# Kernel optimization log

Hardware: AMD Instinct MI355X
Metric: run time of the kernel (lower is better)

Reference implementation:

```python
import jax, jax.numpy as jnp
import numpy as np

P = 16          # patch size
IMG = 384       # image size
D = 768         # model dim
DM = 3072       # mlp hidden
L = 12          # n blocks
H = 12          # n heads
DH = D // H     # head dim
NC = 1000       # n classes
B = 64          # batch
N = (IMG // P) ** 2  # 576 patches


def layernorm(x, w, b, eps=1e-5):
    m = jnp.mean(x, axis=-1, keepdims=True)
    v = jnp.mean((x - m) ** 2, axis=-1, keepdims=True)
    return (x - m) / jnp.sqrt(v + eps) * w + b


def gelu(x):
    return jax.nn.gelu(x, approximate=False)  # torch nn.GELU default (erf)


def setup_inputs() -> dict:
    key = jax.random.key(0)
    ks = iter(jax.random.split(key, 40))
    nrm = lambda shape, s=0.02: jax.random.normal(next(ks), shape, jnp.float32) * s
    return {
        "x": jax.random.normal(next(ks), (B, 3, IMG, IMG), jnp.float32),
        "class_embed": nrm((D,)),
        "pose_embed": nrm((N + 1, D)),
        "proj_w": nrm((3 * P * P, D)), "proj_b": jnp.zeros((D,), jnp.float32),
        "qkv_w": nrm((L, D, 3 * D)), "qkv_b": jnp.zeros((L, 3 * D), jnp.float32),
        "top_w": nrm((L, D, D)), "top_b": jnp.zeros((L, D), jnp.float32),
        "ln1_w": jnp.ones((L, D), jnp.float32), "ln1_b": jnp.zeros((L, D), jnp.float32),
        "ln2_w": jnp.ones((L, D), jnp.float32), "ln2_b": jnp.zeros((L, D), jnp.float32),
        "mlp_w1": nrm((L, D, DM)), "mlp_b1": jnp.zeros((L, DM), jnp.float32),
        "mlp_w2": nrm((L, DM, D)), "mlp_b2": jnp.zeros((L, D), jnp.float32),
        "ln3_w": jnp.ones((D,), jnp.float32), "ln3_b": jnp.zeros((D,), jnp.float32),
        "head_w1": nrm((D, DM)), "head_b1": jnp.zeros((DM,), jnp.float32),
        "head_w2": nrm((DM, NC)), "head_b2": jnp.zeros((NC,), jnp.float32),
    }


def reference(x, class_embed, pose_embed, proj_w, proj_b, qkv_w, qkv_b,
              top_w, top_b, ln1_w, ln1_b, ln2_w, ln2_b,
              mlp_w1, mlp_b1, mlp_w2, mlp_b2, ln3_w, ln3_b,
              head_w1, head_b1, head_w2, head_b2):
    Bx = x.shape[0]
    # _slice_patch: torch unfold(dim2).unfold(dim3) -> (B,C,N,P,P) -> permute -> flatten (C,Ph,Pw order)
    patches = x.reshape(Bx, 3, IMG // P, P, IMG // P, P)
    patches = patches.transpose(0, 2, 4, 1, 3, 5).reshape(Bx, N, 3 * P * P)
    patch_embed = patches @ proj_w + proj_b  # (B, N, D)
    cls = jnp.broadcast_to(class_embed, (Bx, 1, D))
    z = jnp.concatenate([cls, patch_embed], axis=1) + pose_embed  # (B, N+1, D)

    scale = DH ** 0.5
    for i in range(L):
        # MSA branch (note: source computes attention over the HEAD axis per token, HxH)
        h = layernorm(z, ln1_w[i], ln1_b[i])
        qkv = h @ qkv_w[i] + qkv_b[i]
        q, k, v = jnp.split(qkv, 3, axis=-1)
        q = q.reshape(Bx, N + 1, H, DH)
        k = k.reshape(Bx, N + 1, H, DH)
        v = v.reshape(Bx, N + 1, H, DH)
        A = jax.nn.softmax(jnp.einsum('bnhd,bngd->bnhg', q, k) / scale, axis=-1)
        o = jnp.einsum('bnhg,bngd->bnhd', A, v).reshape(Bx, N + 1, D)
        z = o @ top_w[i] + top_b[i] + z
        # MLP branch (GELU after both linears, per source MLP)
        h2 = layernorm(z, ln2_w[i], ln2_b[i])
        m = gelu(gelu(h2 @ mlp_w1[i] + mlp_b1[i]) @ mlp_w2[i] + mlp_b2[i])
        z = m + z

    y = layernorm(z[:, 0], ln3_w, ln3_b)  # (B, D)
    logit = gelu(gelu(y @ head_w1 + head_b1) @ head_w2 + head_b2)  # pretraining cls_head = MLP
    return logit
```

## Files before the change

kernel.cpp:

```cpp
#include <hip/hip_runtime.h>

typedef unsigned short u16;
typedef unsigned int u32;
typedef __bf16 bf16x8 __attribute__((ext_vector_type(8)));
typedef float f32x4 __attribute__((ext_vector_type(4)));

#define D_    768
#define DM_   3072
#define NL_   12
#define NT_   577
#define NP_   576
#define B_    64
#define MREAL (B_*NT_)
#define MPAD2 37120
#define NC_   1000
#define IMG_  384

__device__ __forceinline__ float bf2f(u16 v){
  union { unsigned u; float f; } c; c.u = ((unsigned)v) << 16; return c.f;
}
__device__ __forceinline__ u16 f2bf(float f){
  union { float f; unsigned u; } c; c.f = f;
  unsigned r = c.u + 0x7FFFu + ((c.u >> 16) & 1u);
  return (u16)(r >> 16);
}
__device__ __forceinline__ float gelu_f(float x){
  return 0.5f * x * (1.0f + erff(x * 0.70710678118654752f));
}
__device__ __forceinline__ void gload16(const void* g, void* l){
  __builtin_amdgcn_global_load_lds((const __attribute__((address_space(1))) void*)g,
                                   (__attribute__((address_space(3))) void*)l, 16, 0, 0);
}

template<int EPI>
__global__ __launch_bounds__(512, 1) void gemm256_k(
    const u16* __restrict__ A, const u16* __restrict__ Bt,
    const float* __restrict__ bias, const float* __restrict__ res,
    void* __restrict__ outv, int K, int ldo, int nbn)
{
  __shared__ u16 lds[2][2][256*64];
  const int tid = threadIdx.x;
  const int l   = tid & 63;
  const int wid = tid >> 6;
  const int wm  = wid >> 2, wn = wid & 3;
  const int lrow = l & 15;

  const int nwg = gridDim.x;
  const int q = nwg >> 3, r = nwg & 7;
  const int xcd = blockIdx.x & 7, o = blockIdx.x >> 3;
  const int wg = (xcd < r ? xcd * (q + 1) : r * (q + 1) + (xcd - r) * q) + o;
  const int bm = wg / nbn, bn = wg % nbn;

  const int cs8 = ((tid & 7) ^ ((tid >> 3) & 7)) * 8;
  const int rb  = tid >> 3;
  const u16* aP[4]; const u16* bP[4];
  #pragma unroll
  for (int i = 0; i < 4; i++) {
    aP[i] = A  + (size_t)(bm*256 + rb + 64*i) * K + cs8;
    bP[i] = Bt + (size_t)(bn*256 + rb + 64*i) * K + cs8;
  }
  const int ldst = tid * 8;

  f32x4 acc[8][4];
  #pragma unroll
  for (int i = 0; i < 8; i++)
    #pragma unroll
    for (int j = 0; j < 4; j++) acc[i][j] = {0.f, 0.f, 0.f, 0.f};

  const int nk = K >> 6;
  #pragma unroll
  for (int i = 0; i < 4; i++) {
    gload16(aP[i], &lds[0][0][ldst + i*4096]);
    gload16(bP[i], &lds[0][1][ldst + i*4096]);
    aP[i] += 64; bP[i] += 64;
  }

  const int sw  = (lrow & 7) << 4;
  const int g16 = (l >> 4) << 4;

  for (int t = 0; t < nk; ++t) {
    const int cur = t & 1;
    if (t + 1 < nk) {
      #pragma unroll
      for (int i = 0; i < 4; i++) {
        gload16(aP[i], &lds[cur^1][0][ldst + i*4096]);
        gload16(bP[i], &lds[cur^1][1][ldst + i*4096]);
        aP[i] += 64; bP[i] += 64;
      }
      __builtin_amdgcn_sched_barrier(0);
      asm volatile("s_waitcnt vmcnt(8)" ::: "memory");
    } else {
      __builtin_amdgcn_sched_barrier(0);
      asm volatile("s_waitcnt vmcnt(0)" ::: "memory");
    }
    __builtin_amdgcn_sched_barrier(0);
    __builtin_amdgcn_s_barrier();
    __builtin_amdgcn_sched_barrier(0);
    const char* As_ = (const char*)&lds[cur][0][0];
    const char* Bs_ = (const char*)&lds[cur][1][0];
    #pragma unroll
    for (int kk = 0; kk < 2; kk++) {
      bf16x8 af[8], bfr[4];
      const int kb = (kk << 6) | g16;
      #pragma unroll
      for (int mi = 0; mi < 8; mi++)
        af[mi] = *(const bf16x8*)(As_ + ((wm*128 + mi*16 + lrow) << 7) + (kb ^ sw));
      #pragma unroll
      for (int ni = 0; ni < 4; ni++)
        bfr[ni] = *(const bf16x8*)(Bs_ + ((wn*64 + ni*16 + lrow) << 7) + (kb ^ sw));
      #pragma unroll
      for (int mi = 0; mi < 8; mi++)
        #pragma unroll
        for (int ni = 0; ni < 4; ni++)
          acc[mi][ni] = __builtin_amdgcn_mfma_f32_16x16x32_bf16(af[mi], bfr[ni], acc[mi][ni], 0, 0, 0);
    }
    __builtin_amdgcn_sched_barrier(0);
    __builtin_amdgcn_s_barrier();
    __builtin_amdgcn_sched_barrier(0);
  }

  const int orow0 = bm*256 + wm*128;
  const int ocol0 = bn*256 + wn*64;
  #pragma unroll
  for (int mi = 0; mi < 8; mi++) {
    #pragma unroll
    for (int ni = 0; ni < 4; ni++) {
      const int col = ocol0 + ni*16 + (l & 15);
      const float bv = bias[col];
      #pragma unroll
      for (int r2 = 0; r2 < 4; r2++) {
        const int row = orow0 + mi*16 + (l >> 4)*4 + r2;
        const float v = acc[mi][ni][r2] + bv;
        const size_t idx = (size_t)row * ldo + col;
        if constexpr (EPI == 0) ((u16*)outv)[idx] = f2bf(v);
        else if constexpr (EPI == 1) ((float*)outv)[idx] = v + res[idx];
        else if constexpr (EPI == 2) ((u16*)outv)[idx] = f2bf(gelu_f(v));
        else if constexpr (EPI == 3) ((float*)outv)[idx] = gelu_f(v) + res[idx];
        else if constexpr (EPI == 4) ((float*)outv)[idx] = v;
      }
    }
  }
}

template<int EPI>
__global__ __launch_bounds__(256) void gemm_k(
    const u16* __restrict__ A, const u16* __restrict__ Bt,
    const float* __restrict__ bias, const float* __restrict__ res,
    void* __restrict__ outv, int K, int ldo, int nbn, int Ms, int Ns)
{
  __shared__ u16 As[128*64];
  __shared__ u16 Bs[128*64];
  const int tid = threadIdx.x;
  const int l   = tid & 63;
  const int w   = tid >> 6;
  const int wm  = w >> 1, wn = w & 1;
  const int lrow = l & 15;

  const int nwg = gridDim.x;
  const int q = nwg >> 3, r = nwg & 7;
  const int xcd = blockIdx.x & 7, o = blockIdx.x >> 3;
  const int wg = (xcd < r ? xcd * (q + 1) : r * (q + 1) + (xcd - r) * q) + o;
  const int bm = wg / nbn, bn = wg % nbn;

  const int cs8 = ((tid & 7) ^ ((tid >> 3) & 7)) * 8;
  const int rb  = tid >> 3;
  const size_t abase = (size_t)bm * 128 * K;
  const size_t bbase = (size_t)bn * 128 * K;
  size_t aoff[4], boff[4];
  #pragma unroll
  for (int i = 0; i < 4; i++) {
    aoff[i] = abase + (size_t)(rb + 32 * i) * K + cs8;
    boff[i] = bbase + (size_t)(rb + 32 * i) * K + cs8;
  }

  const int colA = (l >> 4) << 4;
  const int sw   = (lrow & 7) << 4;

  f32x4 acc[4][4];
  #pragma unroll
  for (int i = 0; i < 4; i++)
    #pragma unroll
    for (int j = 0; j < 4; j++) acc[i][j] = {0.f, 0.f, 0.f, 0.f};

  const int nk = K >> 6;
  for (int kt = 0; kt < nk; ++kt) {
    const int koff = kt * 64;
    #pragma unroll
    for (int i = 0; i < 4; i++) {
      gload16(A  + aoff[i] + koff, As + tid * 8 + i * 2048);
      gload16(Bt + boff[i] + koff, Bs + tid * 8 + i * 2048);
    }
    __syncthreads();
    #pragma unroll
    for (int kk = 0; kk < 2; kk++) {
      bf16x8 af[4], bfr[4];
      #pragma unroll
      for (int mi = 0; mi < 4; mi++)
        af[mi] = *(const bf16x8*)((const char*)As +
                  ((wm*64 + mi*16 + lrow) << 7) + (((kk << 6) | colA) ^ sw));
      #pragma unroll
      for (int ni = 0; ni < 4; ni++)
        bfr[ni] = *(const bf16x8*)((const char*)Bs +
                  ((wn*64 + ni*16 + lrow) << 7) + (((kk << 6) | colA) ^ sw));
      #pragma unroll
      for (int mi = 0; mi < 4; mi++)
        #pragma unroll
        for (int ni = 0; ni < 4; ni++)
          acc[mi][ni] = __builtin_amdgcn_mfma_f32_16x16x32_bf16(af[mi], bfr[ni], acc[mi][ni], 0, 0, 0);
    }
    __syncthreads();
  }

  const int orow0 = bm*128 + wm*64;
  const int ocol0 = bn*128 + wn*64;
  #pragma unroll
  for (int mi = 0; mi < 4; mi++) {
    #pragma unroll
    for (int ni = 0; ni < 4; ni++) {
      #pragma unroll
      for (int r2 = 0; r2 < 4; r2++) {
        const int row = orow0 + mi*16 + (l >> 4)*4 + r2;
        const int col = ocol0 + ni*16 + (l & 15);
        float bv;
        if constexpr (EPI == 5) bv = (col < Ns) ? bias[col] : 0.f;
        else bv = bias[col];
        const float v = acc[mi][ni][r2] + bv;
        const size_t idx = (size_t)row * ldo + col;
        if constexpr (EPI == 2) ((u16*)outv)[idx] = f2bf(gelu_f(v));
        else if constexpr (EPI == 5) {
          if (row < Ms && col < Ns) ((float*)outv)[(size_t)row * Ns + col] = gelu_f(v);
        }
      }
    }
  }
}

__global__ void wconv_k(const float* __restrict__ W, u16* __restrict__ Wt,
                        int K, int N)
{
  __shared__ float tile[32][33];
  const int n0 = blockIdx.x * 32, k0 = blockIdx.y * 32;
  const int tx = threadIdx.x, ty = threadIdx.y;
  #pragma unroll
  for (int r = 0; r < 4; r++) {
    const int kk = k0 + ty + r*8;
    const int nn = n0 + tx;
    tile[ty + r*8][tx] = (nn < N) ? W[(size_t)kk * N + nn] : 0.f;
  }
  __syncthreads();
  #pragma unroll
  for (int r = 0; r < 4; r++) {
    const int nn = n0 + ty + r*8;
    Wt[(size_t)nn * K + k0 + tx] = f2bf(tile[tx][ty + r*8]);
  }
}

__global__ void patchify_k(const float* __restrict__ x, u16* __restrict__ hb)
{
  const int blk = blockIdx.x;
  const int b = blk / NP_, p = blk % NP_;
  const int pr = p / 24, pc = p % 24;
  const size_t row = (size_t)b * NT_ + 1 + p;
  #pragma unroll
  for (int u = 0; u < 3; u++) {
    const int j  = threadIdx.x + u * 256;
    const int c  = j >> 8, ph = (j >> 4) & 15, pw = j & 15;
    const float v = x[((size_t)(b*3 + c) * IMG_ + pr*16 + ph) * IMG_ + pc*16 + pw];
    hb[row * D_ + j] = f2bf(v);
  }
}

__global__ void posecls_k(float* __restrict__ z, const float* __restrict__ ce,
                          const float* __restrict__ pe)
{
  const int row = blockIdx.x;
  const int t = row % NT_;
  const size_t base = (size_t)row * D_;
  #pragma unroll
  for (int u = 0; u < 3; u++) {
    const int j = threadIdx.x + u * 256;
    if (t == 0) z[base + j] = ce[j] + pe[j];
    else        z[base + j] += pe[(size_t)t * D_ + j];
  }
}

__global__ void ln_k(const float* __restrict__ z, const float* __restrict__ w,
                     const float* __restrict__ b, u16* __restrict__ out)
{
  const int row = blockIdx.x * 4 + (threadIdx.x >> 6);
  const int l = threadIdx.x & 63;
  const float4* zr = (const float4*)(z + (size_t)row * D_);
  float4 xq[3];
  float s = 0.f;
  #pragma unroll
  for (int j = 0; j < 3; j++) {
    xq[j] = zr[j*64 + l];
    s += xq[j].x + xq[j].y + xq[j].z + xq[j].w;
  }
  #pragma unroll
  for (int m = 1; m < 64; m <<= 1) s += __shfl_xor(s, m, 64);
  const float mean = s * (1.0f / 768.0f);
  float ss = 0.f;
  #pragma unroll
  for (int j = 0; j < 3; j++) {
    const float dx = xq[j].x-mean, dy = xq[j].y-mean, dz = xq[j].z-mean, dw = xq[j].w-mean;
    ss += dx*dx + dy*dy + dz*dz + dw*dw;
  }
  #pragma unroll
  for (int m = 1; m < 64; m <<= 1) ss += __shfl_xor(ss, m, 64);
  const float rinv = rsqrtf(ss * (1.0f / 768.0f) + 1e-5f);
  const size_t ob = (size_t)row * D_;
  #pragma unroll
  for (int j = 0; j < 3; j++) {
    const int c = (j*64 + l) * 4;
    const float4 wv = *(const float4*)(w + c);
    const float4 bv = *(const float4*)(b + c);
    ushort4 ov;
    ov.x = f2bf((xq[j].x - mean) * rinv * wv.x + bv.x);
    ov.y = f2bf((xq[j].y - mean) * rinv * wv.y + bv.y);
    ov.z = f2bf((xq[j].z - mean) * rinv * wv.z + bv.z);
    ov.w = f2bf((xq[j].w - mean) * rinv * wv.w + bv.w);
    *(ushort4*)(out + ob + c) = ov;
  }
}

__global__ void lncls_k(const float* __restrict__ z, const float* __restrict__ w,
                        const float* __restrict__ b, u16* __restrict__ out)
{
  const int row = blockIdx.x * 4 + (threadIdx.x >> 6);
  const int l = threadIdx.x & 63;
  const size_t ob = (size_t)row * D_;
  if (row >= B_) {
    #pragma unroll
    for (int j = 0; j < 12; j++) out[ob + j*64 + l] = 0;
    return;
  }
  const float* zr = z + (size_t)row * NT_ * D_;
  float xv[12];
  float s = 0.f;
  #pragma unroll
  for (int j = 0; j < 12; j++) { xv[j] = zr[j*64 + l]; s += xv[j]; }
  #pragma unroll
  for (int m = 1; m < 64; m <<= 1) s += __shfl_xor(s, m, 64);
  const float mean = s * (1.0f / 768.0f);
  float ss = 0.f;
  #pragma unroll
  for (int j = 0; j < 12; j++) { const float d = xv[j] - mean; ss += d * d; }
  #pragma unroll
  for (int m = 1; m < 64; m <<= 1) ss += __shfl_xor(ss, m, 64);
  const float rinv = rsqrtf(ss * (1.0f / 768.0f) + 1e-5f);
  #pragma unroll
  for (int j = 0; j < 12; j++) {
    const int cidx = j*64 + l;
    out[ob + cidx] = f2bf((xv[j] - mean) * rinv * w[cidx] + b[cidx]);
  }
}

__global__ __launch_bounds__(256) void attn_k(const u16* __restrict__ qkv,
                                              u16* __restrict__ o)
{
  const int tok = (blockIdx.x * 256 + threadIdx.x) >> 6;
  const int l  = threadIdx.x & 63;
  const int g  = l >> 4, li = l & 15;
  const size_t rb = (size_t)tok * (3 * D_);

  f32x4 s = {0.f, 0.f, 0.f, 0.f};
  #pragma unroll
  for (int kt = 0; kt < 2; kt++) {
    const bf16x8 ka = *(const bf16x8*)(qkv + rb + D_ + li*64 + g*8 + kt*32);
    const bf16x8 qb = *(const bf16x8*)(qkv + rb +      li*64 + g*8 + kt*32);
    s = __builtin_amdgcn_mfma_f32_16x16x32_bf16(ka, qb, s, 0, 0, 0);
  }

  float sv[4];
  #pragma unroll
  for (int r2 = 0; r2 < 4; r2++) sv[r2] = s[r2] * 0.125f;
  float mx = (g < 3) ? fmaxf(fmaxf(sv[0], sv[1]), fmaxf(sv[2], sv[3])) : -1e30f;
  mx = fmaxf(mx, __shfl_xor(mx, 16, 64));
  mx = fmaxf(mx, __shfl_xor(mx, 32, 64));
  float p[4], den = 0.f;
  #pragma unroll
  for (int r2 = 0; r2 < 4; r2++) {
    p[r2] = (g < 3) ? __expf(sv[r2] - mx) : 0.f;
    den += p[r2];
  }
  den += __shfl_xor(den, 16, 64);
  den += __shfl_xor(den, 32, 64);
  const float rden = 1.0f / den;
  #pragma unroll
  for (int r2 = 0; r2 < 4; r2++) p[r2] *= rden;

  const u32 pk01 = ((u32)f2bf(p[1]) << 16) | f2bf(p[0]);
  const u32 pk23 = ((u32)f2bf(p[3]) << 16) | f2bf(p[2]);

  const int srcA = (li + (g << 5)) & 63;
  const int srcB = (srcA + 16) & 63;
  u32 b0 = (u32)__shfl((int)pk01, srcA, 64);
  u32 b1 = (u32)__shfl((int)pk23, srcA, 64);
  u32 b2 = (u32)__shfl((int)pk01, srcB, 64);
  u32 b3 = (u32)__shfl((int)pk23, srcB, 64);
  if (g >= 2) { b0 = 0; b1 = 0; b2 = 0; b3 = 0; }
  union { u32 u[4]; bf16x8 v; } pb;
  pb.u[0] = b0; pb.u[1] = b1; pb.u[2] = b2; pb.u[3] = b3;

  const size_t ob = (size_t)tok * D_;
  #pragma unroll
  for (int t = 0; t < 4; t++) {
    union { u16 a[8]; bf16x8 v; } va;
    #pragma unroll
    for (int jp = 0; jp < 8; jp++) {
      const int j = g * 8 + jp;
      va.a[jp] = (j < 12) ? qkv[rb + 2*D_ + j*64 + t*16 + li] : (u16)0;
    }
    f32x4 oac = {0.f, 0.f, 0.f, 0.f};
    oac = __builtin_amdgcn_mfma_f32_16x16x32_bf16(va.v, pb.v, oac, 0, 0, 0);
    if (li < 12) {
      ushort4 ov;
      ov.x = f2bf(oac[0]); ov.y = f2bf(oac[1]);
      ov.z = f2bf(oac[2]); ov.w = f2bf(oac[3]);
      *(ushort4*)(o + ob + li*64 + t*16 + g*4) = ov;
    }
  }
}

extern "C" void kernel_launch(void* const* d_in, const int* in_sizes, int n_in,
                              void* d_out, int out_size, void* d_ws, size_t ws_size,
                              hipStream_t stream)
{
  const float* x    = (const float*)d_in[0];
  const float* ce   = (const float*)d_in[1];
  const float* pe   = (const float*)d_in[2];
  const float* pw   = (const float*)d_in[3];
  const float* pb   = (const float*)d_in[4];
  const float* qkvw = (const float*)d_in[5];
  const float* qkvb = (const float*)d_in[6];
  const float* topw = (const float*)d_in[7];
  const float* topb = (const float*)d_in[8];
  const float* l1w  = (const float*)d_in[9];
  const float* l1b  = (const float*)d_in[10];
  const float* l2w  = (const float*)d_in[11];
  const float* l2b  = (const float*)d_in[12];
  const float* w1   = (const float*)d_in[13];
  const float* b1   = (const float*)d_in[14];
  const float* w2   = (const float*)d_in[15];
  const float* b2   = (const float*)d_in[16];
  const float* l3w  = (const float*)d_in[17];
  const float* l3b  = (const float*)d_in[18];
  const float* hw1  = (const float*)d_in[19];
  const float* hb1  = (const float*)d_in[20];
  const float* hw2  = (const float*)d_in[21];
  const float* hb2  = (const float*)d_in[22];

  char* ws = (char*)d_ws;
  constexpr size_t SZ_Z  = (size_t)MPAD2 * D_ * 4;
  constexpr size_t SZ_HB = (size_t)MPAD2 * D_ * 2;
  constexpr size_t SZ_QM = (size_t)MPAD2 * DM_ * 2;
  constexpr size_t SZ_WB = (size_t)DM_ * 1024 * 2;
  constexpr size_t SZ_YB = (size_t)128 * D_ * 2;
  float* z  = (float*)ws;
  u16*   hb = (u16*)(ws + SZ_Z);
  u16*   qm = (u16*)(ws + SZ_Z + SZ_HB);
  u16*   wb = (u16*)(ws + SZ_Z + SZ_HB + SZ_QM);
  u16*   yb = (u16*)(ws + SZ_Z + SZ_HB + SZ_QM + SZ_WB);
  u16*   t1 = (u16*)(ws + SZ_Z + SZ_HB + SZ_QM + SZ_WB + SZ_YB);

  const dim3 blk(256);
  const dim3 blk5(512);
  const dim3 wblk(32, 8);
  const int MT2 = MPAD2 / 256;

  patchify_k<<<B_ * NP_, blk, 0, stream>>>(x, hb);
  wconv_k<<<dim3(D_/32, D_/32), wblk, 0, stream>>>(pw, wb, D_, D_);
  gemm256_k<4><<<3*MT2, blk5, 0, stream>>>(hb, wb, pb, nullptr, z, D_, D_, 3);
  posecls_k<<<MREAL, blk, 0, stream>>>(z, ce, pe);

  for (int i = 0; i < NL_; i++) {
    ln_k<<<MPAD2/4, blk, 0, stream>>>(z, l1w + i*D_, l1b + i*D_, hb);
    wconv_k<<<dim3(3*D_/32, D_/32), wblk, 0, stream>>>(qkvw + (size_t)i*D_*3*D_, wb, D_, 3*D_);
    gemm256_k<0><<<9*MT2, blk5, 0, stream>>>(hb, wb, qkvb + i*3*D_, nullptr, qm, D_, 3*D_, 9);
    attn_k<<<MREAL/4, blk, 0, stream>>>(qm, hb);
    wconv_k<<<dim3(D_/32, D_/32), wblk, 0, stream>>>(topw + (size_t)i*D_*D_, wb, D_, D_);
    gemm256_k<1><<<3*MT2, blk5, 0, stream>>>(hb, wb, topb + i*D_, z, z, D_, D_, 3);
    ln_k<<<MPAD2/4, blk, 0, stream>>>(z, l2w + i*D_, l2b + i*D_, hb);
    wconv_k<<<dim3(DM_/32, D_/32), wblk, 0, stream>>>(w1 + (size_t)i*D_*DM_, wb, D_, DM_);
    gemm256_k<2><<<12*MT2, blk5, 0, stream>>>(hb, wb, b1 + i*DM_, nullptr, qm, D_, DM_, 12);
    wconv_k<<<dim3(D_/32, DM_/32), wblk, 0, stream>>>(w2 + (size_t)i*DM_*D_, wb, DM_, D_);
    gemm256_k<3><<<3*MT2, blk5, 0, stream>>>(qm, wb, b2 + i*D_, z, z, DM_, D_, 3);
  }

  lncls_k<<<32, blk, 0, stream>>>(z, l3w, l3b, yb);
  wconv_k<<<dim3(DM_/32, D_/32), wblk, 0, stream>>>(hw1, wb, D_, DM_);
  gemm_k<2><<<24, blk, 0, stream>>>(yb, wb, hb1, nullptr, t1, D_, DM_, 24, 0, 0);
  wconv_k<<<dim3(1024/32, DM_/32), wblk, 0, stream>>>(hw2, wb, DM_, NC_);
  gemm_k<5><<<8, blk, 0, stream>>>(t1, wb, hb2, nullptr, (float*)d_out, DM_, 1024, 8, B_, NC_);
}
```

Measured before the change: 11.85 ms.

## Interleave global prefetch with MFMA phases in GEMM main loop

The GEMM K-loop is split into four sub-phases, each of two M-halves by two K-halves. Each phase loads its A/B fragments from LDS and issues part of the next tile's global-to-LDS prefetch, then raises wave priority around its MFMA block. The aim is to spread memory traffic across the compute, overlap it better, and reduce fragment register pressure (af goes from 8 to 4). The trade-off is four workgroup barriers per K-step instead of two, plus stricter lgkmcnt waits, which could add synchronisation stalls.

```diff
diff --git a/kernel.cpp b/kernel.cpp
--- a/kernel.cpp
+++ b/kernel.cpp
@@ -32,6 +32,8 @@
                                    (__attribute__((address_space(3))) void*)l, 16, 0, 0);
 }
 
+#define SB_ __builtin_amdgcn_sched_barrier(0)
+
 template<int EPI>
 __global__ __launch_bounds__(512, 1) void gemm256_k(
     const u16* __restrict__ A, const u16* __restrict__ Bt,
@@ -80,43 +82,119 @@
 
   for (int t = 0; t < nk; ++t) {
     const int cur = t & 1;
-    if (t + 1 < nk) {
-      #pragma unroll
-      for (int i = 0; i < 4; i++) {
-        gload16(aP[i], &lds[cur^1][0][ldst + i*4096]);
-        gload16(bP[i], &lds[cur^1][1][ldst + i*4096]);
-        aP[i] += 64; bP[i] += 64;
-      }
-      __builtin_amdgcn_sched_barrier(0);
-      asm volatile("s_waitcnt vmcnt(8)" ::: "memory");
-    } else {
-      __builtin_amdgcn_sched_barrier(0);
-      asm volatile("s_waitcnt vmcnt(0)" ::: "memory");
-    }
-    __builtin_amdgcn_sched_barrier(0);
+    const bool pre = (t + 1 < nk);
+    u16* dA = &lds[cur^1][0][0];
+    u16* dB = &lds[cur^1][1][0];
+
+    if (pre) {
+      gload16(aP[0], dA + ldst);
+      gload16(aP[1], dA + ldst + 4096);
+    }
+    SB_;
+    if (pre) asm volatile("s_waitcnt vmcnt(2)" ::: "memory");
+    else     asm volatile("s_waitcnt vmcnt(0)" ::: "memory");
+    SB_;
     __builtin_amdgcn_s_barrier();
-    __builtin_amdgcn_sched_barrier(0);
+    SB_;
+
     const char* As_ = (const char*)&lds[cur][0][0];
     const char* Bs_ = (const char*)&lds[cur][1][0];
-    #pragma unroll
-    for (int kk = 0; kk < 2; kk++) {
-      bf16x8 af[8], bfr[4];
-      const int kb = (kk << 6) | g16;
-      #pragma unroll
-      for (int mi = 0; mi < 8; mi++)
-        af[mi] = *(const bf16x8*)(As_ + ((wm*128 + mi*16 + lrow) << 7) + (kb ^ sw));
+    bf16x8 af[4], bfr[4];
+
+    {
+      const int kb = g16;
       #pragma unroll
       for (int ni = 0; ni < 4; ni++)
         bfr[ni] = *(const bf16x8*)(Bs_ + ((wn*64 + ni*16 + lrow) << 7) + (kb ^ sw));
       #pragma unroll
-      for (int mi = 0; mi < 8; mi++)
+      for (int mi = 0; mi < 4; mi++)
+        af[mi] = *(const bf16x8*)(As_ + ((wm*128 + mi*16 + lrow) << 7) + (kb ^ sw));
+      if (pre) {
+        gload16(aP[2], dA + ldst + 8192);
+        gload16(aP[3], dA + ldst + 12288);
+      }
+      asm volatile("s_waitcnt lgkmcnt(0)" ::: "memory");
+      SB_;
+      __builtin_amdgcn_s_setprio(1);
+      #pragma unroll
+      for (int mi = 0; mi < 4; mi++)
         #pragma unroll
         for (int ni = 0; ni < 4; ni++)
           acc[mi][ni] = __builtin_amdgcn_mfma_f32_16x16x32_bf16(af[mi], bfr[ni], acc[mi][ni], 0, 0, 0);
-    }
-    __builtin_amdgcn_sched_barrier(0);
-    __builtin_amdgcn_s_barrier();
-    __builtin_amdgcn_sched_barrier(0);
+      __builtin_amdgcn_s_setprio(0);
+      SB_;
+      __builtin_amdgcn_s_barrier();
+      SB_;
+    }
+    {
+      const int kb = g16;
+      #pragma unroll
+      for (int mi = 0; mi < 4; mi++)
+        af[mi] = *(const bf16x8*)(As_ + ((wm*128 + (mi+4)*16 + lrow) << 7) + (kb ^ sw));
+      if (pre) {
+        gload16(bP[0], dB + ldst);
+        gload16(bP[1], dB + ldst + 4096);
+      }
+      asm volatile("s_waitcnt lgkmcnt(0)" ::: "memory");
+      SB_;
+      __builtin_amdgcn_s_setprio(1);
+      #pragma unroll
+      for (int mi = 0; mi < 4; mi++)
+        #pragma unroll
+        for (int ni = 0; ni < 4; ni++)
+          acc[mi+4][ni] = __builtin_amdgcn_mfma_f32_16x16x32_bf16(af[mi], bfr[ni], acc[mi+4][ni], 0, 0, 0);
+      __builtin_amdgcn_s_setprio(0);
+      SB_;
+      __builtin_amdgcn_s_barrier();
+      SB_;
+    }
+    {
+      const int kb = 64 | g16;
+      #pragma unroll
+      for (int ni = 0; ni < 4; ni++)
+        bfr[ni] = *(const bf16x8*)(Bs_ + ((wn*64 + ni*16 + lrow) << 7) + (kb ^ sw));
+      #pragma unroll
+      for (int mi = 0; mi < 4; mi++)
+        af[mi] = *(const bf16x8*)(As_ + ((wm*128 + mi*16 + lrow) << 7) + (kb ^ sw));
+      if (pre) {
+        gload16(bP[2], dB + ldst + 8192);
+        gload16(bP[3], dB + ldst + 12288);
+      }
+      asm volatile("s_waitcnt lgkmcnt(0)" ::: "memory");
+      SB_;
+      __builtin_amdgcn_s_setprio(1);
+      #pragma unroll
+      for (int mi = 0; mi < 4; mi++)
+        #pragma unroll
+        for (int ni = 0; ni < 4; ni++)
+          acc[mi][ni] = __builtin_amdgcn_mfma_f32_16x16x32_bf16(af[mi], bfr[ni], acc[mi][ni], 0, 0, 0);
+      __builtin_amdgcn_s_setprio(0);
+      SB_;
+      __builtin_amdgcn_s_barrier();
+      SB_;
+    }
+    {
+      const int kb = 64 | g16;
+      #pragma unroll
+      for (int mi = 0; mi < 4; mi++)
+        af[mi] = *(const bf16x8*)(As_ + ((wm*128 + (mi+4)*16 + lrow) << 7) + (kb ^ sw));
+      asm volatile("s_waitcnt lgkmcnt(0)" ::: "memory");
+      SB_;
+      __builtin_amdgcn_s_setprio(1);
+      #pragma unroll
+      for (int mi = 0; mi < 4; mi++)
+        #pragma unroll
+        for (int ni = 0; ni < 4; ni++)
+          acc[mi+4][ni] = __builtin_amdgcn_mfma_f32_16x16x32_bf16(af[mi], bfr[ni], acc[mi+4][ni], 0, 0, 0);
+      __builtin_amdgcn_s_setprio(0);
+      SB_;
+      __builtin_amdgcn_s_barrier();
+      SB_;
+    }
+    if (pre) {
+      #pragma unroll
+      for (int i = 0; i < 4; i++) { aP[i] += 64; bP[i] += 64; }
+    }
   }
 
   const int orow0 = bm*256 + wm*128;
```

Measured after the change: 11.24 ms. 5.2% less time.

## Add 128x128 GEMM kernel for N=768 projections and raise MFMA priority

Applied to the files above, without the earlier changes.

Adds a 128x128-tile, 256-thread GEMM variant with two workgroups per CU and uses it for the patch embedding, attention output projection and MLP down-projection, where N=768 produced only 3 column tiles and a small grid. The 256-tile kernel is kept for the QKV and MLP up-projections, now without the residual epilogues. Both kernels replace the sched_barrier-wrapped barriers with a plain inline s_barrier and raise wave priority around the MFMA section with s_setprio. Smaller tiles give more workgroups and better CU fill, at the cost of lower data reuse per tile and more global traffic. Dropping the sched_barriers lets the compiler move instructions around the waits.

```diff
diff --git a/kernel.cpp b/kernel.cpp
--- a/kernel.cpp
+++ b/kernel.cpp
@@ -31,11 +31,16 @@
   __builtin_amdgcn_global_load_lds((const __attribute__((address_space(1))) void*)g,
                                    (__attribute__((address_space(3))) void*)l, 16, 0, 0);
 }
+#define BAR_ asm volatile("s_barrier" ::: "memory")
+
+__device__ __forceinline__ void epi_store(int EPI, void* outv, const float* res,
+                                          size_t idx, float v){
+}
 
 template<int EPI>
 __global__ __launch_bounds__(512, 1) void gemm256_k(
     const u16* __restrict__ A, const u16* __restrict__ Bt,
-    const float* __restrict__ bias, const float* __restrict__ res,
+    const float* __restrict__ bias,
     void* __restrict__ outv, int K, int ldo, int nbn)
 {
   __shared__ u16 lds[2][2][256*64];
@@ -87,17 +92,14 @@
         gload16(bP[i], &lds[cur^1][1][ldst + i*4096]);
         aP[i] += 64; bP[i] += 64;
       }
-      __builtin_amdgcn_sched_barrier(0);
       asm volatile("s_waitcnt vmcnt(8)" ::: "memory");
     } else {
-      __builtin_amdgcn_sched_barrier(0);
       asm volatile("s_waitcnt vmcnt(0)" ::: "memory");
     }
-    __builtin_amdgcn_sched_barrier(0);
-    __builtin_amdgcn_s_barrier();
-    __builtin_amdgcn_sched_barrier(0);
+    BAR_;
     const char* As_ = (const char*)&lds[cur][0][0];
     const char* Bs_ = (const char*)&lds[cur][1][0];
+    __builtin_amdgcn_s_setprio(1);
     #pragma unroll
     for (int kk = 0; kk < 2; kk++) {
       bf16x8 af[8], bfr[4];
@@ -114,9 +116,8 @@
         for (int ni = 0; ni < 4; ni++)
           acc[mi][ni] = __builtin_amdgcn_mfma_f32_16x16x32_bf16(af[mi], bfr[ni], acc[mi][ni], 0, 0, 0);
     }
-    __builtin_amdgcn_sched_barrier(0);
-    __builtin_amdgcn_s_barrier();
-    __builtin_amdgcn_sched_barrier(0);
+    __builtin_amdgcn_s_setprio(0);
+    BAR_;
   }
 
   const int orow0 = bm*256 + wm*128;
@@ -133,8 +134,109 @@
         const float v = acc[mi][ni][r2] + bv;
         const size_t idx = (size_t)row * ldo + col;
         if constexpr (EPI == 0) ((u16*)outv)[idx] = f2bf(v);
-        else if constexpr (EPI == 1) ((float*)outv)[idx] = v + res[idx];
         else if constexpr (EPI == 2) ((u16*)outv)[idx] = f2bf(gelu_f(v));
+      }
+    }
+  }
+}
+
+template<int EPI>
+__global__ __launch_bounds__(256, 2) void gemm128_k(
+    const u16* __restrict__ A, const u16* __restrict__ Bt,
+    const float* __restrict__ bias, const float* __restrict__ res,
+    void* __restrict__ outv, int K, int ldo, int nbn)
+{
+  __shared__ u16 lds[2][2][128*64];
+  const int tid = threadIdx.x;
+  const int l   = tid & 63;
+  const int w   = tid >> 6;
+  const int wm  = w >> 1, wn = w & 1;
+  const int lrow = l & 15;
+
+  const int nwg = gridDim.x;
+  const int q = nwg >> 3, r = nwg & 7;
+  const int xcd = blockIdx.x & 7, o = blockIdx.x >> 3;
+  const int wg = (xcd < r ? xcd * (q + 1) : r * (q + 1) + (xcd - r) * q) + o;
+  const int bm = wg / nbn, bn = wg % nbn;
+
+  const int cs8 = ((tid & 7) ^ ((tid >> 3) & 7)) * 8;
+  const int rb  = tid >> 3;
+  const u16* aP[4]; const u16* bP[4];
+  #pragma unroll
+  for (int i = 0; i < 4; i++) {
+    aP[i] = A  + (size_t)(bm*128 + rb + 32*i) * K + cs8;
+    bP[i] = Bt + (size_t)(bn*128 + rb + 32*i) * K + cs8;
+  }
+  const int ldst = tid * 8;
+
+  f32x4 acc[4][4];
+  #pragma unroll
+  for (int i = 0; i < 4; i++)
+    #pragma unroll
+    for (int j = 0; j < 4; j++) acc[i][j] = {0.f, 0.f, 0.f, 0.f};
+
+  const int nk = K >> 6;
+  #pragma unroll
+  for (int i = 0; i < 4; i++) {
+    gload16(aP[i], &lds[0][0][ldst + i*2048]);
+    gload16(bP[i], &lds[0][1][ldst + i*2048]);
+    aP[i] += 64; bP[i] += 64;
+  }
+
+  const int sw  = (lrow & 7) << 4;
+  const int g16 = (l >> 4) << 4;
+
+  for (int t = 0; t < nk; ++t) {
+    const int cur = t & 1;
+    if (t + 1 < nk) {
+      #pragma unroll
+      for (int i = 0; i < 4; i++) {
+        gload16(aP[i], &lds[cur^1][0][ldst + i*2048]);
+        gload16(bP[i], &lds[cur^1][1][ldst + i*2048]);
+        aP[i] += 64; bP[i] += 64;
+      }
+      asm volatile("s_waitcnt vmcnt(8)" ::: "memory");
+    } else {
+      asm volatile("s_waitcnt vmcnt(0)" ::: "memory");
+    }
+    BAR_;
+    const char* As_ = (const char*)&lds[cur][0][0];
+    const char* Bs_ = (const char*)&lds[cur][1][0];
+    __builtin_amdgcn_s_setprio(1);
+    #pragma unroll
+    for (int kk = 0; kk < 2; kk++) {
+      bf16x8 af[4], bfr[4];
+      const int kb = (kk << 6) | g16;
+      #pragma unroll
+      for (int mi = 0; mi < 4; mi++)
+        af[mi] = *(const bf16x8*)(As_ + ((wm*64 + mi*16 + lrow) << 7) + (kb ^ sw));
+      #pragma unroll
+      for (int ni = 0; ni < 4; ni++)
+        bfr[ni] = *(const bf16x8*)(Bs_ + ((wn*64 + ni*16 + lrow) << 7) + (kb ^ sw));
+      #pragma unroll
+      for (int mi = 0; mi < 4; mi++)
+        #pragma unroll
+        for (int ni = 0; ni < 4; ni++)
+          acc[mi][ni] = __builtin_amdgcn_mfma_f32_16x16x32_bf16(af[mi], bfr[ni], acc[mi][ni], 0, 0, 0);
+    }
+    __builtin_amdgcn_s_setprio(0);
+    BAR_;
+  }
+
+  const int orow0 = bm*128 + wm*64;
+  const int ocol0 = bn*128 + wn*64;
+  #pragma unroll
+  for (int mi = 0; mi < 4; mi++) {
+    #pragma unroll
+    for (int ni = 0; ni < 4; ni++) {
+      const int col = ocol0 + ni*16 + (l & 15);
+      const float bv = bias[col];
+      #pragma unroll
+      for (int r2 = 0; r2 < 4; r2++) {
+        const int row = orow0 + mi*16 + (l >> 4)*4 + r2;
+        const float v = acc[mi][ni][r2] + bv;
+        const size_t idx = (size_t)row * ldo + col;
+        if constexpr (EPI == 1) ((float*)outv)[idx] = v + res[idx];
         else if constexpr (EPI == 3) ((float*)outv)[idx] = gelu_f(v) + res[idx];
         else if constexpr (EPI == 4) ((float*)outv)[idx] = v;
       }
@@ -467,25 +569,26 @@
   const dim3 blk(256);
   const dim3 blk5(512);
   const dim3 wblk(32, 8);
+  const int MT1 = MPAD2 / 128;
   const int MT2 = MPAD2 / 256;
 
   patchify_k<<<B_ * NP_, blk, 0, stream>>>(x, hb);
   wconv_k<<<dim3(D_/32, D_/32), wblk, 0, stream>>>(pw, wb, D_, D_);
-  gemm256_k<4><<<3*MT2, blk5, 0, stream>>>(hb, wb, pb, nullptr, z, D_, D_, 3);
+  gemm128_k<4><<<6*MT1, blk, 0, stream>>>(hb, wb, pb, nullptr, z, D_, D_, 6);
   posecls_k<<<MREAL, blk, 0, stream>>>(z, ce, pe);
 
   for (int i = 0; i < NL_; i++) {
     ln_k<<<MPAD2/4, blk, 0, stream>>>(z, l1w + i*D_, l1b + i*D_, hb);
     wconv_k<<<dim3(3*D_/32, D_/32), wblk, 0, stream>>>(qkvw + (size_t)i*D_*3*D_, wb, D_, 3*D_);
-    gemm256_k<0><<<9*MT2, blk5, 0, stream>>>(hb, wb, qkvb + i*3*D_, nullptr, qm, D_, 3*D_, 9);
+    gemm256_k<0><<<9*MT2, blk5, 0, stream>>>(hb, wb, qkvb + i*3*D_, qm, D_, 3*D_, 9);
     attn_k<<<MREAL/4, blk, 0, stream>>>(qm, hb);
     wconv_k<<<dim3(D_/32, D_/32), wblk, 0, stream>>>(topw + (size_t)i*D_*D_, wb, D_, D_);
-    gemm256_k<1><<<3*MT2, blk5, 0, stream>>>(hb, wb, topb + i*D_, z, z, D_, D_, 3);
+    gemm128_k<1><<<6*MT1, blk, 0, stream>>>(hb, wb, topb + i*D_, z, z, D_, D_, 6);
     ln_k<<<MPAD2/4, blk, 0, stream>>>(z, l2w + i*D_, l2b + i*D_, hb);
     wconv_k<<<dim3(DM_/32, D_/32), wblk, 0, stream>>>(w1 + (size_t)i*D_*DM_, wb, D_, DM_);
-    gemm256_k<2><<<12*MT2, blk5, 0, stream>>>(hb, wb, b1 + i*DM_, nullptr, qm, D_, DM_, 12);
+    gemm256_k<2><<<12*MT2, blk5, 0, stream>>>(hb, wb, b1 + i*DM_, qm, D_, DM_, 12);
     wconv_k<<<dim3(D_/32, DM_/32), wblk, 0, stream>>>(w2 + (size_t)i*DM_*D_, wb, DM_, D_);
-    gemm256_k<3><<<3*MT2, blk5, 0, stream>>>(qm, wb, b2 + i*D_, z, z, DM_, D_, 3);
+    gemm128_k<3><<<6*MT1, blk, 0, stream>>>(qm, wb, b2 + i*D_, z, z, DM_, D_, 6);
   }
 
   lncls_k<<<32, blk, 0, stream>>>(z, l3w, l3b, yb);
```

After: 11.61 ms. 2.1% less time.

## Restructure main GEMM into eight-phase pipelined schedule with split K-halves

Applied to the files above, without the earlier changes.

Replaces the double-buffered 256x256 GEMM main loop with an eight-phase schedule. Each K tile is split into 32-wide halves held in separate LDS buffers, and each phase issues a small batch of global-to-LDS loads interleaved with half of the MFMA work. It also changes the LDS layout to pair rows with a 4-way XOR swizzle and raises wave priority around MFMA bursts. The aim is to overlap memory traffic with compute more finely and cut stall time at barriers, at the cost of many more barriers and fragile vmcnt accounting that assumes K is a multiple of 128.

```diff
diff --git a/kernel.cpp b/kernel.cpp
--- a/kernel.cpp
+++ b/kernel.cpp
@@ -33,12 +33,12 @@
 }
 
 template<int EPI>
-__global__ __launch_bounds__(512, 1) void gemm256_k(
+__global__ __launch_bounds__(512, 1) void gemm8p_k(
     const u16* __restrict__ A, const u16* __restrict__ Bt,
     const float* __restrict__ bias, const float* __restrict__ res,
     void* __restrict__ outv, int K, int ldo, int nbn)
 {
-  __shared__ u16 lds[2][2][256*64];
+  __shared__ u16 lds[8][8192];
   const int tid = threadIdx.x;
   const int l   = tid & 63;
   const int wid = tid >> 6;
@@ -51,15 +51,25 @@
   const int wg = (xcd < r ? xcd * (q + 1) : r * (q + 1) + (xcd - r) * q) + o;
   const int bm = wg / nbn, bn = wg % nbn;
 
-  const int cs8 = ((tid & 7) ^ ((tid >> 3) & 7)) * 8;
-  const int rb  = tid >> 3;
-  const u16* aP[4]; const u16* bP[4];
-  #pragma unroll
-  for (int i = 0; i < 4; i++) {
-    aP[i] = A  + (size_t)(bm*256 + rb + 64*i) * K + cs8;
-    bP[i] = Bt + (size_t)(bn*256 + rb + 64*i) * K + cs8;
-  }
-  const int ldst = tid * 8;
+  const int Rrow = 2 * (tid >> 3) + ((tid >> 2) & 1);
+  const int c16s = (tid & 3) ^ ((tid >> 3) & 3);
+  const u16* aS0 = A  + (size_t)(bm*256 + Rrow) * K + c16s * 8;
+  const u16* aS1 = aS0 + (size_t)128 * K;
+  const u16* bS0 = Bt + (size_t)(bn*256 + Rrow) * K + c16s * 8;
+  const u16* bS1 = bS0 + (size_t)128 * K;
+  const int dstb = tid * 16;
+
+  int afo[8], bfo[4];
+  #pragma unroll
+  for (int mi = 0; mi < 8; mi++) {
+    const int R = wm*128 + mi*16 + lrow;
+    afo[mi] = (R >> 1)*128 + (R & 1)*64 + (((l >> 4) ^ ((R >> 1) & 3)) << 4);
+  }
+  #pragma unroll
+  for (int ni = 0; ni < 4; ni++) {
+    const int R = wn*64 + ni*16 + lrow;
+    bfo[ni] = (R >> 1)*128 + (R & 1)*64 + (((l >> 4) ^ ((R >> 1) & 3)) << 4);
+  }
 
   f32x4 acc[8][4];
   #pragma unroll
@@ -67,56 +77,70 @@
     #pragma unroll
     for (int j = 0; j < 4; j++) acc[i][j] = {0.f, 0.f, 0.f, 0.f};
 
-  const int nk = K >> 6;
-  #pragma unroll
-  for (int i = 0; i < 4; i++) {
-    gload16(aP[i], &lds[0][0][ldst + i*4096]);
-    gload16(bP[i], &lds[0][1][ldst + i*4096]);
-    aP[i] += 64; bP[i] += 64;
-  }
-
-  const int sw  = (lrow & 7) << 4;
-  const int g16 = (l >> 4) << 4;
-
-  for (int t = 0; t < nk; ++t) {
-    const int cur = t & 1;
-    if (t + 1 < nk) {
-      #pragma unroll
-      for (int i = 0; i < 4; i++) {
-        gload16(aP[i], &lds[cur^1][0][ldst + i*4096]);
-        gload16(bP[i], &lds[cur^1][1][ldst + i*4096]);
-        aP[i] += 64; bP[i] += 64;
-      }
-      __builtin_amdgcn_sched_barrier(0);
-      asm volatile("s_waitcnt vmcnt(8)" ::: "memory");
-    } else {
-      __builtin_amdgcn_sched_barrier(0);
-      asm volatile("s_waitcnt vmcnt(0)" ::: "memory");
-    }
-    __builtin_amdgcn_sched_barrier(0);
-    __builtin_amdgcn_s_barrier();
-    __builtin_amdgcn_sched_barrier(0);
-    const char* As_ = (const char*)&lds[cur][0][0];
-    const char* Bs_ = (const char*)&lds[cur][1][0];
-    #pragma unroll
-    for (int kk = 0; kk < 2; kk++) {
-      bf16x8 af[8], bfr[4];
-      const int kb = (kk << 6) | g16;
-      #pragma unroll
-      for (int mi = 0; mi < 8; mi++)
-        af[mi] = *(const bf16x8*)(As_ + ((wm*128 + mi*16 + lrow) << 7) + (kb ^ sw));
-      #pragma unroll
-      for (int ni = 0; ni < 4; ni++)
-        bfr[ni] = *(const bf16x8*)(Bs_ + ((wn*64 + ni*16 + lrow) << 7) + (kb ^ sw));
-      #pragma unroll
-      for (int mi = 0; mi < 8; mi++)
-        #pragma unroll
-        for (int ni = 0; ni < 4; ni++)
-          acc[mi][ni] = __builtin_amdgcn_mfma_f32_16x16x32_bf16(af[mi], bfr[ni], acc[mi][ni], 0, 0, 0);
-    }
-    __builtin_amdgcn_sched_barrier(0);
-    __builtin_amdgcn_s_barrier();
-    __builtin_amdgcn_sched_barrier(0);
+  const int nk  = K >> 6;
+  const int nit = nk >> 1;
+
+#define STG(t_, kk_, ab_) { \
+    const u16* s0_ = ((ab_) ? bS0 : aS0) + (t_)*64 + (kk_)*32; \
+    const u16* s1_ = ((ab_) ? bS1 : aS1) + (t_)*64 + (kk_)*32; \
+    char* d_ = (char*)&lds[(((t_)&1)<<2) | ((kk_)<<1) | (ab_)][0]; \
+    gload16(s0_, d_ + dstb); \
+    gload16(s1_, d_ + dstb + 8192); }
+
+#define PH_READS(As_, Bs_, mh_, rb_) { \
+    if (rb_) { \
+      _Pragma("unroll") \
+      for (int n_ = 0; n_ < 4; n_++) \
+        bfr[n_] = *(const bf16x8*)((const char*)&lds[Bs_][0] + bfo[n_]); \
+    } \
+    _Pragma("unroll") \
+    for (int m_ = 0; m_ < 4; m_++) \
+      af[m_] = *(const bf16x8*)((const char*)&lds[As_][0] + afo[(mh_)*4 + m_]); }
+
+#define PH_MFMA(mh_) { \
+    __builtin_amdgcn_s_setprio(1); \
+    _Pragma("unroll") \
+    for (int m_ = 0; m_ < 4; m_++) \
+      _Pragma("unroll") \
+      for (int n_ = 0; n_ < 4; n_++) \
+        acc[(mh_)*4 + m_][n_] = __builtin_amdgcn_mfma_f32_16x16x32_bf16(af[m_], bfr[n_], acc[(mh_)*4 + m_][n_], 0, 0, 0); \
+    __builtin_amdgcn_s_setprio(0); }
+
+#define BARX __builtin_amdgcn_s_barrier()
+#define VMW(n_) asm volatile("s_waitcnt vmcnt(" #n_ ")" ::: "memory")
+
+  STG(0,0,0); STG(0,0,1); STG(0,1,0); STG(0,1,1); STG(1,0,0); STG(1,0,1);
+  VMW(8);
+  BARX;
+
+  for (int i = 0; i < nit; ++i) {
+    const int t1 = 2*i + 1, t2 = 2*i + 2, t3 = 2*i + 3;
+    const bool lastI = (i == nit - 1);
+    bf16x8 af[4], bfr[4];
+
+    PH_READS(0, 1, 0, 1); STG(t1,1,0);
+    BARX; PH_MFMA(0); BARX;
+    PH_READS(0, 1, 1, 0); STG(t1,1,1);
+    BARX; PH_MFMA(1);
+    VMW(8); BARX;
+    PH_READS(2, 3, 0, 1); if (!lastI) { STG(t2,0,0); }
+    BARX; PH_MFMA(0); BARX;
+    PH_READS(2, 3, 1, 0); if (!lastI) { STG(t2,0,1); }
+    BARX; PH_MFMA(1);
+    if (lastI) { VMW(4); } else { VMW(8); }
+    BARX;
+    PH_READS(4, 5, 0, 1); if (!lastI) { STG(t2,1,0); }
+    BARX; PH_MFMA(0); BARX;
+    PH_READS(4, 5, 1, 0); if (!lastI) { STG(t2,1,1); }
+    BARX; PH_MFMA(1);
+    if (lastI) { VMW(0); } else { VMW(8); }
+    BARX;
+    PH_READS(6, 7, 0, 1); if (!lastI) { STG(t3,0,0); }
+    BARX; PH_MFMA(0); BARX;
+    PH_READS(6, 7, 1, 0); if (!lastI) { STG(t3,0,1); }
+    BARX; PH_MFMA(1);
+    if (!lastI) { VMW(8); }
+    BARX;
   }
 
   const int orow0 = bm*256 + wm*128;
@@ -140,6 +164,11 @@
       }
     }
   }
+#undef STG
+#undef PH_READS
+#undef PH_MFMA
+#undef BARX
+#undef VMW
 }
 
 template<int EPI>
@@ -471,21 +500,21 @@
 
   patchify_k<<<B_ * NP_, blk, 0, stream>>>(x, hb);
   wconv_k<<<dim3(D_/32, D_/32), wblk, 0, stream>>>(pw, wb, D_, D_);
-  gemm256_k<4><<<3*MT2, blk5, 0, stream>>>(hb, wb, pb, nullptr, z, D_, D_, 3);
+  gemm8p_k<4><<<3*MT2, blk5, 0, stream>>>(hb, wb, pb, nullptr, z, D_, D_, 3);
   posecls_k<<<MREAL, blk, 0, stream>>>(z, ce, pe);
 
   for (int i = 0; i < NL_; i++) {
     ln_k<<<MPAD2/4, blk, 0, stream>>>(z, l1w + i*D_, l1b + i*D_, hb);
     wconv_k<<<dim3(3*D_/32, D_/32), wblk, 0, stream>>>(qkvw + (size_t)i*D_*3*D_, wb, D_, 3*D_);
-    gemm256_k<0><<<9*MT2, blk5, 0, stream>>>(hb, wb, qkvb + i*3*D_, nullptr, qm, D_, 3*D_, 9);
+    gemm8p_k<0><<<9*MT2, blk5, 0, stream>>>(hb, wb, qkvb + i*3*D_, nullptr, qm, D_, 3*D_, 9);
     attn_k<<<MREAL/4, blk, 0, stream>>>(qm, hb);
     wconv_k<<<dim3(D_/32, D_/32), wblk, 0, stream>>>(topw + (size_t)i*D_*D_, wb, D_, D_);
-    gemm256_k<1><<<3*MT2, blk5, 0, stream>>>(hb, wb, topb + i*D_, z, z, D_, D_, 3);
+    gemm8p_k<1><<<3*MT2, blk5, 0, stream>>>(hb, wb, topb + i*D_, z, z, D_, D_, 3);
     ln_k<<<MPAD2/4, blk, 0, stream>>>(z, l2w + i*D_, l2b + i*D_, hb);
     wconv_k<<<dim3(DM_/32, D_/32), wblk, 0, stream>>>(w1 + (size_t)i*D_*DM_, wb, D_, DM_);
-    gemm256_k<2><<<12*MT2, blk5, 0, stream>>>(hb, wb, b1 + i*DM_, nullptr, qm, D_, DM_, 12);
+    gemm8p_k<2><<<12*MT2, blk5, 0, stream>>>(hb, wb, b1 + i*DM_, nullptr, qm, D_, DM_, 12);
     wconv_k<<<dim3(D_/32, DM_/32), wblk, 0, stream>>>(w2 + (size_t)i*DM_*D_, wb, DM_, D_);
-    gemm256_k<3><<<3*MT2, blk5, 0, stream>>>(qm, wb, b2 + i*D_, z, z, DM_, D_, 3);
+    gemm8p_k<3><<<3*MT2, blk5, 0, stream>>>(qm, wb, b2 + i*D_, z, z, DM_, D_, 3);
   }
 
   lncls_k<<<32, blk, 0, stream>>>(z, l3w, l3b, yb);
```

Result: faster. 11.42 ms (-3.6%).
